# Kernel tuning notes

Hardware: AMD Instinct MI355X
Metric: run time of the kernel (lower is better)

Reference implementation:

```python
import jax, jax.numpy as jnp
import numpy as np

MAX_ITER = 10
EPS = 1e-4


def setup_inputs() -> dict:
    key = jax.random.key(0)
    k1, k2, k3 = jax.random.split(key, 3)
    B, N, M = 64, 1024, 1024
    s = jax.random.uniform(k1, (B, N, M), dtype=jnp.float32)
    nrows = jax.random.randint(k2, (B,), 0, N, dtype=jnp.int64 if jax.config.read('jax_enable_x64') else jnp.int32)
    ncols = jax.random.randint(k3, (B,), 0, M, dtype=nrows.dtype)
    return {"s": s, "nrows": nrows, "ncols": ncols}


def _sinkhorn(s, nrows, ncols):
    # Faithful to torch Sinkhorn.forward with exp=False, dummy_row=False.
    # The torch code builds [B,N,N]/[B,M,M] block-of-ones matrices and matmuls;
    # mathematically this is a masked column-sum (even iters) / row-sum (odd iters)
    # over the valid nrows[b] x ncols[b] block, followed by division inside the
    # block and zeroing outside it.
    B, N, M = s.shape
    row_mask = jnp.arange(N)[None, :] < nrows[:, None]            # [B, N]
    col_mask = jnp.arange(M)[None, :] < ncols[:, None]            # [B, M]
    mask = row_mask[:, :, None] & col_mask[:, None, :]            # [B, N, M]

    out = s + EPS
    for i in range(MAX_ITER):
        if i % 2 == 0:
            # column sums over valid rows -> [B, 1, M]
            sm = jnp.sum(jnp.where(row_mask[:, :, None], out, 0.0), axis=1, keepdims=True)
        else:
            # row sums over valid cols -> [B, N, 1]
            sm = jnp.sum(jnp.where(col_mask[:, None, :], out, 0.0), axis=2, keepdims=True)
        sm = jnp.where(sm == 0, 1.0, sm)  # guard (only affects masked-out entries)
        out = jnp.where(mask, out / sm, 0.0)
    return out


def reference(s, nrows, ncols):
    return _sinkhorn(s, nrows, ncols)
```

## Files before the change

kernel.cpp:

```cpp
#include <hip/hip_runtime.h>

#define EPS 1e-4f
constexpr int N_DIM = 1024;
constexpr int M_DIM = 1024;
constexpr int BATCH = 64;


template <bool FIRST, int CHUNKS>
__global__ __launch_bounds__(256)
void col_sweep(const float* __restrict__ s,
               const int* __restrict__ nrows,
               const int* __restrict__ ncols,
               const float* __restrict__ u,
               float* __restrict__ tpart) {
    const int b  = blockIdx.y;
    const int mt = blockIdx.x & 3;
    const int ch = blockIdx.x >> 2;
    const int R = nrows[b], C = ncols[b];
    const int lane = threadIdx.x & 63, wv = threadIdx.x >> 6;
    const int m0 = mt * 256;
    const int m  = m0 + lane * 4;

    constexpr int ROWS = N_DIM / CHUNKS;
    const int n0 = ch * ROWS;
    const int nend = min(R, n0 + ROWS);

    __shared__ float rlds[1024];
    if (!FIRST) {
        for (int i = threadIdx.x; i < ROWS; i += 256) {
            float uu = u[b * N_DIM + n0 + i];
            rlds[i] = (uu == 0.f) ? 1.f : 1.f / uu;
        }
        __syncthreads();
    }

    float4 acc = make_float4(0.f, 0.f, 0.f, 0.f);
    if (m0 < C) {
        const float* __restrict__ sb = s + (size_t)b * N_DIM * M_DIM;
#pragma unroll 4
        for (int n = n0 + wv; n < nend; n += 4) {
            float4 v = *(const float4*)(sb + (size_t)n * M_DIM + m);
            float rn = FIRST ? 1.f : rlds[n - n0];
            acc.x += rn * (v.x + EPS);
            acc.y += rn * (v.y + EPS);
            acc.z += rn * (v.z + EPS);
            acc.w += rn * (v.w + EPS);
        }
    }

    __shared__ float4 red[4][64];
    red[wv][lane] = acc;
    __syncthreads();
    if (wv == 0) {
        float4 a0 = red[0][lane], a1 = red[1][lane],
               a2 = red[2][lane], a3 = red[3][lane];
        float4 t = make_float4(a0.x + a1.x + a2.x + a3.x,
                               a0.y + a1.y + a2.y + a3.y,
                               a0.z + a1.z + a2.z + a3.z,
                               a0.w + a1.w + a2.w + a3.w);
        *(float4*)(tpart + ((size_t)(ch * BATCH + b)) * M_DIM + m) = t;
    }
}

template <int CHUNKS, bool WRITE_C>
__global__ __launch_bounds__(256)
void row_sweep(const float* __restrict__ s,
               const int* __restrict__ nrows,
               const int* __restrict__ ncols,
               const float* __restrict__ tpart,
               float* __restrict__ u,
               float* __restrict__ cOut) {
    const int b = blockIdx.y;
    const int R = nrows[b], C = ncols[b];
    const int n0 = blockIdx.x * 16;
    if (n0 >= R) return;

    __shared__ float clds[M_DIM];
    {
        const int t4 = threadIdx.x;
        float4 sum = make_float4(0.f, 0.f, 0.f, 0.f);
#pragma unroll
        for (int ch = 0; ch < CHUNKS; ++ch) {
            float4 p = *(const float4*)(tpart + ((size_t)(ch * BATCH + b)) * M_DIM + t4 * 4);
            sum.x += p.x; sum.y += p.y; sum.z += p.z; sum.w += p.w;
        }
        float4 cv;
        cv.x = (sum.x == 0.f) ? 1.f : 1.f / sum.x;
        cv.y = (sum.y == 0.f) ? 1.f : 1.f / sum.y;
        cv.z = (sum.z == 0.f) ? 1.f : 1.f / sum.z;
        cv.w = (sum.w == 0.f) ? 1.f : 1.f / sum.w;
        *(float4*)&clds[t4 * 4] = cv;
        if (WRITE_C && blockIdx.x == 0)
            *(float4*)(cOut + b * M_DIM + t4 * 4) = cv;
    }
    __syncthreads();

    const int lane = threadIdx.x & 63, wv = threadIdx.x >> 6;
    const int C4 = C >> 2;
#pragma unroll
    for (int i = 0; i < 4; ++i) {
        const int n = n0 + wv * 4 + i;
        if (n >= R) break;
        const float* __restrict__ srow = s + ((size_t)b * N_DIM + n) * M_DIM;
        float sum = 0.f;
        for (int j = lane; j < C4; j += 64) {
            float4 v  = ((const float4*)srow)[j];
            float4 cc = *(const float4*)&clds[j * 4];
            sum += (v.x + EPS) * cc.x + (v.y + EPS) * cc.y +
                   (v.z + EPS) * cc.z + (v.w + EPS) * cc.w;
        }
        for (int mm = (C4 << 2) + lane; mm < C; mm += 64)
            sum += (srow[mm] + EPS) * clds[mm];
#pragma unroll
        for (int off = 32; off; off >>= 1) sum += __shfl_down(sum, off);
        if (lane == 0) u[b * N_DIM + n] = sum;
    }
}

__global__ __launch_bounds__(256)
void finalize(const float* __restrict__ s,
              const int* __restrict__ nrows,
              const int* __restrict__ ncols,
              const float* __restrict__ u,
              const float* __restrict__ c,
              float* __restrict__ out) {
    const int n = blockIdx.x;
    const int b = blockIdx.y;
    const int R = nrows[b], C = ncols[b];
    const size_t base = ((size_t)b * N_DIM + n) * M_DIM;
    const int m = threadIdx.x * 4;

    float4 o = make_float4(0.f, 0.f, 0.f, 0.f);
    if (n < R && m < C) {
        float uu = u[b * N_DIM + n];
        float rn = (uu == 0.f) ? 1.f : 1.f / uu;
        float4 v  = *(const float4*)(s + base + m);
        float4 cc = *(const float4*)(c + b * M_DIM + m);
        o.x = (m + 0 < C) ? (v.x + EPS) * rn * cc.x : 0.f;
        o.y = (m + 1 < C) ? (v.y + EPS) * rn * cc.y : 0.f;
        o.z = (m + 2 < C) ? (v.z + EPS) * rn * cc.z : 0.f;
        o.w = (m + 3 < C) ? (v.w + EPS) * rn * cc.w : 0.f;
    }
    *(float4*)(out + base + m) = o;
}

extern "C" void kernel_launch(void* const* d_in, const int* in_sizes, int n_in,
                              void* d_out, int out_size, void* d_ws, size_t ws_size,
                              hipStream_t stream) {
    const float* s     = (const float*)d_in[0];
    const int*   nrows = (const int*)d_in[1];
    const int*   ncols = (const int*)d_in[2];
    float*       out   = (float*)d_out;

    const size_t needed4 = (size_t)(4 * BATCH * M_DIM + BATCH * N_DIM + BATCH * M_DIM) * 4;
    const bool big = ws_size >= needed4;

    if (big) {
        constexpr int CH = 4;
        float* tpart = (float*)d_ws;
        float* u = tpart + (size_t)CH * BATCH * M_DIM;
        float* c = u + (size_t)BATCH * N_DIM;
        dim3 colGrid(4 * CH, BATCH), rowGrid(64, BATCH);
        col_sweep<true, CH><<<colGrid, 256, 0, stream>>>(s, nrows, ncols, u, tpart);
        row_sweep<CH, false><<<rowGrid, 256, 0, stream>>>(s, nrows, ncols, tpart, u, c);
        for (int k = 1; k < 4; ++k) {
            col_sweep<false, CH><<<colGrid, 256, 0, stream>>>(s, nrows, ncols, u, tpart);
            row_sweep<CH, false><<<rowGrid, 256, 0, stream>>>(s, nrows, ncols, tpart, u, c);
        }
        col_sweep<false, CH><<<colGrid, 256, 0, stream>>>(s, nrows, ncols, u, tpart);
        row_sweep<CH, true><<<rowGrid, 256, 0, stream>>>(s, nrows, ncols, tpart, u, c);
        finalize<<<dim3(N_DIM, BATCH), 256, 0, stream>>>(s, nrows, ncols, u, c, out);
    } else {
        constexpr int CH = 1;
        float* tpart = (float*)d_ws;
        float* u = tpart + (size_t)CH * BATCH * M_DIM;
        float* c = u + (size_t)BATCH * N_DIM;
        dim3 colGrid(4 * CH, BATCH), rowGrid(64, BATCH);
        col_sweep<true, CH><<<colGrid, 256, 0, stream>>>(s, nrows, ncols, u, tpart);
        row_sweep<CH, false><<<rowGrid, 256, 0, stream>>>(s, nrows, ncols, tpart, u, c);
        for (int k = 1; k < 4; ++k) {
            col_sweep<false, CH><<<colGrid, 256, 0, stream>>>(s, nrows, ncols, u, tpart);
            row_sweep<CH, false><<<rowGrid, 256, 0, stream>>>(s, nrows, ncols, tpart, u, c);
        }
        col_sweep<false, CH><<<colGrid, 256, 0, stream>>>(s, nrows, ncols, u, tpart);
        row_sweep<CH, true><<<rowGrid, 256, 0, stream>>>(s, nrows, ncols, tpart, u, c);
        finalize<<<dim3(N_DIM, BATCH), 256, 0, stream>>>(s, nrows, ncols, u, c, out);
    }
}
```

Baseline: 244.3 us.

## Cache fp16 copy of masked input and run Sinkhorn sweeps on it

The first column sweep adds EPS, masks columns, and writes a half-precision copy of the input into the workspace. All later row and column sweeps read this fp16 copy instead of the fp32 input, halving the bytes per sweep. Row blocks and column blocks are widened to 8 elements per lane. The cost is an extra write pass, a large workspace requirement, and fp16 rounding error in the normalisation sums.

```diff
diff --git a/kernel.cpp b/kernel.cpp
--- a/kernel.cpp
+++ b/kernel.cpp
@@ -1,17 +1,216 @@
 #include <hip/hip_runtime.h>
+#include <hip/hip_fp16.h>
 
 #define EPS 1e-4f
 constexpr int N_DIM = 1024;
 constexpr int M_DIM = 1024;
 constexpr int BATCH = 64;
-
+constexpr int CH    = 4;
+constexpr int ROWS  = N_DIM / CH;
+
+
+
+__global__ __launch_bounds__(256)
+void col_first_conv(const float* __restrict__ s,
+                    const int* __restrict__ nrows,
+                    const int* __restrict__ ncols,
+                    __half* __restrict__ h,
+                    float* __restrict__ tpart) {
+    const int b  = blockIdx.y;
+    const int mt = blockIdx.x & 3;
+    const int ch = blockIdx.x >> 2;
+    const int R = nrows[b], C = ncols[b];
+    const int lane = threadIdx.x & 63, wv = threadIdx.x >> 6;
+    const int m = mt * 256 + lane * 4;
+    const int n0 = ch * ROWS;
+    const int nend = min(R, n0 + ROWS);
+    const size_t base = (size_t)b * N_DIM * M_DIM;
+
+    float4 acc = make_float4(0.f, 0.f, 0.f, 0.f);
+    if (mt * 256 < C) {
+        for (int n = n0 + wv; n < nend; n += 4) {
+            float4 v = *(const float4*)(s + base + (size_t)n * M_DIM + m);
+            v.x = (m + 0 < C) ? v.x + EPS : 0.f;
+            v.y = (m + 1 < C) ? v.y + EPS : 0.f;
+            v.z = (m + 2 < C) ? v.z + EPS : 0.f;
+            v.w = (m + 3 < C) ? v.w + EPS : 0.f;
+            acc.x += v.x; acc.y += v.y; acc.z += v.z; acc.w += v.w;
+            union { __half2 h2[2]; uint2 u2; } pk;
+            pk.h2[0] = __floats2half2_rn(v.x, v.y);
+            pk.h2[1] = __floats2half2_rn(v.z, v.w);
+            *(uint2*)(h + base + (size_t)n * M_DIM + m) = pk.u2;
+        }
+    } else {
+        const uint2 z = make_uint2(0u, 0u);
+        for (int n = n0 + wv; n < nend; n += 4)
+            *(uint2*)(h + base + (size_t)n * M_DIM + m) = z;
+    }
+    __shared__ float4 red[4][64];
+    red[wv][lane] = acc;
+    __syncthreads();
+    if (wv == 0) {
+        float4 a0 = red[0][lane], a1 = red[1][lane],
+               a2 = red[2][lane], a3 = red[3][lane];
+        float4 t = make_float4(a0.x + a1.x + a2.x + a3.x,
+                               a0.y + a1.y + a2.y + a3.y,
+                               a0.z + a1.z + a2.z + a3.z,
+                               a0.w + a1.w + a2.w + a3.w);
+        *(float4*)(tpart + (size_t)(ch * BATCH + b) * M_DIM + m) = t;
+    }
+}
+
+__global__ __launch_bounds__(256)
+void col_h(const __half* __restrict__ h,
+           const int* __restrict__ nrows,
+           const int* __restrict__ ncols,
+           const float* __restrict__ u,
+           float* __restrict__ tpart) {
+    const int b  = blockIdx.y;
+    const int mt = blockIdx.x & 1;
+    const int ch = blockIdx.x >> 1;
+    const int R = nrows[b], C = ncols[b];
+    const int lane = threadIdx.x & 63, wv = threadIdx.x >> 6;
+    const int m = mt * 512 + lane * 8;
+    const int n0 = ch * ROWS;
+    const int nend = min(R, n0 + ROWS);
+    const size_t base = (size_t)b * N_DIM * M_DIM;
+
+    __shared__ float rlds[ROWS];
+    {
+        float uu = u[b * N_DIM + n0 + threadIdx.x];
+        rlds[threadIdx.x] = (uu == 0.f) ? 1.f : 1.f / uu;
+    }
+    __syncthreads();
+
+    float acc[8] = {0.f, 0.f, 0.f, 0.f, 0.f, 0.f, 0.f, 0.f};
+    if (mt * 512 < C) {
+        for (int n = n0 + wv; n < nend; n += 4) {
+            uint4 raw = *(const uint4*)(h + base + (size_t)n * M_DIM + m);
+            const float rn = rlds[n - n0];
+            const __half2* hp = (const __half2*)&raw;
+#pragma unroll
+            for (int k = 0; k < 4; ++k) {
+                float2 f = __half22float2(hp[k]);
+                acc[2 * k]     += rn * f.x;
+                acc[2 * k + 1] += rn * f.y;
+            }
+        }
+    }
+    __shared__ float red[4][64 * 8];
+#pragma unroll
+    for (int k = 0; k < 8; ++k) red[wv][lane * 8 + k] = acc[k];
+    __syncthreads();
+    if (wv == 0) {
+        float t[8];
+#pragma unroll
+        for (int k = 0; k < 8; ++k)
+            t[k] = red[0][lane * 8 + k] + red[1][lane * 8 + k] +
+                   red[2][lane * 8 + k] + red[3][lane * 8 + k];
+        float* tp = tpart + (size_t)(ch * BATCH + b) * M_DIM + m;
+        *(float4*)tp       = make_float4(t[0], t[1], t[2], t[3]);
+        *(float4*)(tp + 4) = make_float4(t[4], t[5], t[6], t[7]);
+    }
+}
+
+template <bool WRITE_C>
+__global__ __launch_bounds__(256)
+void row_h(const __half* __restrict__ h,
+           const int* __restrict__ nrows,
+           const int* __restrict__ ncols,
+           const float* __restrict__ tpart,
+           float* __restrict__ u,
+           float* __restrict__ cOut) {
+    const int b = blockIdx.y;
+    const int R = nrows[b], C = ncols[b];
+    const int n0 = blockIdx.x * 32;
+    if (n0 >= R) return;
+    const size_t base = (size_t)b * N_DIM * M_DIM;
+
+    __shared__ float clds[M_DIM];
+    {
+        const int t4 = threadIdx.x * 4;
+        float4 sum = make_float4(0.f, 0.f, 0.f, 0.f);
+#pragma unroll
+        for (int ch = 0; ch < CH; ++ch) {
+            float4 p = *(const float4*)(tpart + (size_t)(ch * BATCH + b) * M_DIM + t4);
+            sum.x += p.x; sum.y += p.y; sum.z += p.z; sum.w += p.w;
+        }
+        float4 cv;
+        cv.x = (sum.x == 0.f) ? 1.f : 1.f / sum.x;
+        cv.y = (sum.y == 0.f) ? 1.f : 1.f / sum.y;
+        cv.z = (sum.z == 0.f) ? 1.f : 1.f / sum.z;
+        cv.w = (sum.w == 0.f) ? 1.f : 1.f / sum.w;
+        *(float4*)&clds[t4] = cv;
+        if (WRITE_C && blockIdx.x == 0)
+            *(float4*)(cOut + b * M_DIM + t4) = cv;
+    }
+    __syncthreads();
+
+    const int lane = threadIdx.x & 63, wv = threadIdx.x >> 6;
+    const bool hi = (C > 512);
+#pragma unroll 2
+    for (int i = 0; i < 8; ++i) {
+        const int n = n0 + wv * 8 + i;
+        if (n >= R) break;
+        const __half* hrow = h + base + (size_t)n * M_DIM;
+        float sum = 0.f;
+        {
+            uint4 raw = *(const uint4*)(hrow + lane * 8);
+            const __half2* hp = (const __half2*)&raw;
+            const float* cl = &clds[lane * 8];
+#pragma unroll
+            for (int k = 0; k < 4; ++k) {
+                float2 f = __half22float2(hp[k]);
+                sum += f.x * cl[2 * k] + f.y * cl[2 * k + 1];
+            }
+        }
+        if (hi) {
+            uint4 raw = *(const uint4*)(hrow + 512 + lane * 8);
+            const __half2* hp = (const __half2*)&raw;
+            const float* cl = &clds[512 + lane * 8];
+#pragma unroll
+            for (int k = 0; k < 4; ++k) {
+                float2 f = __half22float2(hp[k]);
+                sum += f.x * cl[2 * k] + f.y * cl[2 * k + 1];
+            }
+        }
+#pragma unroll
+        for (int off = 32; off; off >>= 1) sum += __shfl_down(sum, off);
+        if (lane == 0) u[b * N_DIM + n] = sum;
+    }
+}
+
+__global__ __launch_bounds__(256)
+void finalize(const float* __restrict__ s,
+              const int* __restrict__ nrows,
+              const int* __restrict__ ncols,
+              const float* __restrict__ u,
+              const float* __restrict__ c,
+              float* __restrict__ out) {
+    const int n = blockIdx.x;
+    const int b = blockIdx.y;
+    const int R = nrows[b], C = ncols[b];
+    const size_t base = ((size_t)b * N_DIM + n) * M_DIM;
+    const int m = threadIdx.x * 4;
+
+    float4 o = make_float4(0.f, 0.f, 0.f, 0.f);
+    if (n < R && m < C) {
+        float uu = u[b * N_DIM + n];
+        float rn = (uu == 0.f) ? 1.f : 1.f / uu;
+        float4 v  = *(const float4*)(s + base + m);
+        float4 cc = *(const float4*)(c + b * M_DIM + m);
+        o.x = (m + 0 < C) ? (v.x + EPS) * rn * cc.x : 0.f;
+        o.y = (m + 1 < C) ? (v.y + EPS) * rn * cc.y : 0.f;
+        o.z = (m + 2 < C) ? (v.z + EPS) * rn * cc.z : 0.f;
+        o.w = (m + 3 < C) ? (v.w + EPS) * rn * cc.w : 0.f;
+    }
+    *(float4*)(out + base + m) = o;
+}
 
 template <bool FIRST, int CHUNKS>
 __global__ __launch_bounds__(256)
-void col_sweep(const float* __restrict__ s,
-               const int* __restrict__ nrows,
-               const int* __restrict__ ncols,
-               const float* __restrict__ u,
+void col_sweep(const float* __restrict__ s, const int* __restrict__ nrows,
+               const int* __restrict__ ncols, const float* __restrict__ u,
                float* __restrict__ tpart) {
     const int b  = blockIdx.y;
     const int mt = blockIdx.x & 3;
@@ -20,20 +219,18 @@
     const int lane = threadIdx.x & 63, wv = threadIdx.x >> 6;
     const int m0 = mt * 256;
     const int m  = m0 + lane * 4;
-
-    constexpr int ROWS = N_DIM / CHUNKS;
-    const int n0 = ch * ROWS;
-    const int nend = min(R, n0 + ROWS);
-
-    __shared__ float rlds[1024];
+    constexpr int RW = N_DIM / CHUNKS;
+    const int n0 = ch * RW;
+    const int nend = min(R, n0 + RW);
+
+    __shared__ float rlds[RW > 1024 ? 1 : RW];
     if (!FIRST) {
-        for (int i = threadIdx.x; i < ROWS; i += 256) {
+        for (int i = threadIdx.x; i < RW; i += 256) {
             float uu = u[b * N_DIM + n0 + i];
             rlds[i] = (uu == 0.f) ? 1.f : 1.f / uu;
         }
         __syncthreads();
     }
-
     float4 acc = make_float4(0.f, 0.f, 0.f, 0.f);
     if (m0 < C) {
         const float* __restrict__ sb = s + (size_t)b * N_DIM * M_DIM;
@@ -41,40 +238,31 @@
         for (int n = n0 + wv; n < nend; n += 4) {
             float4 v = *(const float4*)(sb + (size_t)n * M_DIM + m);
             float rn = FIRST ? 1.f : rlds[n - n0];
-            acc.x += rn * (v.x + EPS);
-            acc.y += rn * (v.y + EPS);
-            acc.z += rn * (v.z + EPS);
-            acc.w += rn * (v.w + EPS);
-        }
-    }
-
+            acc.x += rn * (v.x + EPS); acc.y += rn * (v.y + EPS);
+            acc.z += rn * (v.z + EPS); acc.w += rn * (v.w + EPS);
+        }
+    }
     __shared__ float4 red[4][64];
     red[wv][lane] = acc;
     __syncthreads();
     if (wv == 0) {
         float4 a0 = red[0][lane], a1 = red[1][lane],
                a2 = red[2][lane], a3 = red[3][lane];
-        float4 t = make_float4(a0.x + a1.x + a2.x + a3.x,
-                               a0.y + a1.y + a2.y + a3.y,
-                               a0.z + a1.z + a2.z + a3.z,
-                               a0.w + a1.w + a2.w + a3.w);
+        float4 t = make_float4(a0.x + a1.x + a2.x + a3.x, a0.y + a1.y + a2.y + a3.y,
+                               a0.z + a1.z + a2.z + a3.z, a0.w + a1.w + a2.w + a3.w);
         *(float4*)(tpart + ((size_t)(ch * BATCH + b)) * M_DIM + m) = t;
     }
 }
 
 template <int CHUNKS, bool WRITE_C>
 __global__ __launch_bounds__(256)
-void row_sweep(const float* __restrict__ s,
-               const int* __restrict__ nrows,
-               const int* __restrict__ ncols,
-               const float* __restrict__ tpart,
-               float* __restrict__ u,
-               float* __restrict__ cOut) {
+void row_sweep(const float* __restrict__ s, const int* __restrict__ nrows,
+               const int* __restrict__ ncols, const float* __restrict__ tpart,
+               float* __restrict__ u, float* __restrict__ cOut) {
     const int b = blockIdx.y;
     const int R = nrows[b], C = ncols[b];
     const int n0 = blockIdx.x * 16;
     if (n0 >= R) return;
-
     __shared__ float clds[M_DIM];
     {
         const int t4 = threadIdx.x;
@@ -94,7 +282,6 @@
             *(float4*)(cOut + b * M_DIM + t4 * 4) = cv;
     }
     __syncthreads();
-
     const int lane = threadIdx.x & 63, wv = threadIdx.x >> 6;
     const int C4 = C >> 2;
 #pragma unroll
@@ -117,33 +304,6 @@
     }
 }
 
-__global__ __launch_bounds__(256)
-void finalize(const float* __restrict__ s,
-              const int* __restrict__ nrows,
-              const int* __restrict__ ncols,
-              const float* __restrict__ u,
-              const float* __restrict__ c,
-              float* __restrict__ out) {
-    const int n = blockIdx.x;
-    const int b = blockIdx.y;
-    const int R = nrows[b], C = ncols[b];
-    const size_t base = ((size_t)b * N_DIM + n) * M_DIM;
-    const int m = threadIdx.x * 4;
-
-    float4 o = make_float4(0.f, 0.f, 0.f, 0.f);
-    if (n < R && m < C) {
-        float uu = u[b * N_DIM + n];
-        float rn = (uu == 0.f) ? 1.f : 1.f / uu;
-        float4 v  = *(const float4*)(s + base + m);
-        float4 cc = *(const float4*)(c + b * M_DIM + m);
-        o.x = (m + 0 < C) ? (v.x + EPS) * rn * cc.x : 0.f;
-        o.y = (m + 1 < C) ? (v.y + EPS) * rn * cc.y : 0.f;
-        o.z = (m + 2 < C) ? (v.z + EPS) * rn * cc.z : 0.f;
-        o.w = (m + 3 < C) ? (v.w + EPS) * rn * cc.w : 0.f;
-    }
-    *(float4*)(out + base + m) = o;
-}
-
 extern "C" void kernel_launch(void* const* d_in, const int* in_sizes, int n_in,
                               void* d_out, int out_size, void* d_ws, size_t ws_size,
                               hipStream_t stream) {
@@ -152,38 +312,60 @@
     const int*   ncols = (const int*)d_in[2];
     float*       out   = (float*)d_out;
 
-    const size_t needed4 = (size_t)(4 * BATCH * M_DIM + BATCH * N_DIM + BATCH * M_DIM) * 4;
-    const bool big = ws_size >= needed4;
-
-    if (big) {
-        constexpr int CH = 4;
+    const size_t hElems   = (size_t)BATCH * N_DIM * M_DIM;
+    const size_t need_f16 = hElems * 2 +
+                            ((size_t)CH * BATCH * M_DIM + BATCH * N_DIM + BATCH * M_DIM) * 4;
+
+    if (ws_size >= need_f16) {
+        __half* h     = (__half*)d_ws;
+        float*  tpart = (float*)(h + hElems);
+        float*  u     = tpart + (size_t)CH * BATCH * M_DIM;
+        float*  c     = u + (size_t)BATCH * N_DIM;
+
+        dim3 colGrid1(4 * CH, BATCH);
+        dim3 colGridH(2 * CH, BATCH);
+        dim3 rowGridH(32, BATCH);
+
+        col_first_conv<<<colGrid1, 256, 0, stream>>>(s, nrows, ncols, h, tpart);
+        row_h<false><<<rowGridH, 256, 0, stream>>>(h, nrows, ncols, tpart, u, c);
+        for (int k = 0; k < 3; ++k) {
+            col_h<<<colGridH, 256, 0, stream>>>(h, nrows, ncols, u, tpart);
+            row_h<false><<<rowGridH, 256, 0, stream>>>(h, nrows, ncols, tpart, u, c);
+        }
+        col_h<<<colGridH, 256, 0, stream>>>(h, nrows, ncols, u, tpart);
+        row_h<true><<<rowGridH, 256, 0, stream>>>(h, nrows, ncols, tpart, u, c);
+        finalize<<<dim3(N_DIM, BATCH), 256, 0, stream>>>(s, nrows, ncols, u, c, out);
+        return;
+    }
+
+    const size_t need4 = (size_t)(4 * BATCH * M_DIM + BATCH * N_DIM + BATCH * M_DIM) * 4;
+    if (ws_size >= need4) {
         float* tpart = (float*)d_ws;
-        float* u = tpart + (size_t)CH * BATCH * M_DIM;
+        float* u = tpart + (size_t)4 * BATCH * M_DIM;
         float* c = u + (size_t)BATCH * N_DIM;
-        dim3 colGrid(4 * CH, BATCH), rowGrid(64, BATCH);
-        col_sweep<true, CH><<<colGrid, 256, 0, stream>>>(s, nrows, ncols, u, tpart);
-        row_sweep<CH, false><<<rowGrid, 256, 0, stream>>>(s, nrows, ncols, tpart, u, c);
+        dim3 colGrid(16, BATCH), rowGrid(64, BATCH);
+        col_sweep<true, 4><<<colGrid, 256, 0, stream>>>(s, nrows, ncols, u, tpart);
+        row_sweep<4, false><<<rowGrid, 256, 0, stream>>>(s, nrows, ncols, tpart, u, c);
         for (int k = 1; k < 4; ++k) {
-            col_sweep<false, CH><<<colGrid, 256, 0, stream>>>(s, nrows, ncols, u, tpart);
-            row_sweep<CH, false><<<rowGrid, 256, 0, stream>>>(s, nrows, ncols, tpart, u, c);
-        }
-        col_sweep<false, CH><<<colGrid, 256, 0, stream>>>(s, nrows, ncols, u, tpart);
-        row_sweep<CH, true><<<rowGrid, 256, 0, stream>>>(s, nrows, ncols, tpart, u, c);
+            col_sweep<false, 4><<<colGrid, 256, 0, stream>>>(s, nrows, ncols, u, tpart);
+            row_sweep<4, false><<<rowGrid, 256, 0, stream>>>(s, nrows, ncols, tpart, u, c);
+        }
+        col_sweep<false, 4><<<colGrid, 256, 0, stream>>>(s, nrows, ncols, u, tpart);
+        row_sweep<4, true><<<rowGrid, 256, 0, stream>>>(s, nrows, ncols, tpart, u, c);
         finalize<<<dim3(N_DIM, BATCH), 256, 0, stream>>>(s, nrows, ncols, u, c, out);
     } else {
-        constexpr int CH = 1;
         float* tpart = (float*)d_ws;
-        float* u = tpart + (size_t)CH * BATCH * M_DIM;
+        float* u = tpart + (size_t)BATCH * M_DIM;
         float* c = u + (size_t)BATCH * N_DIM;
-        dim3 colGrid(4 * CH, BATCH), rowGrid(64, BATCH);
-        col_sweep<true, CH><<<colGrid, 256, 0, stream>>>(s, nrows, ncols, u, tpart);
-        row_sweep<CH, false><<<rowGrid, 256, 0, stream>>>(s, nrows, ncols, tpart, u, c);
+        dim3 colGrid(4, BATCH), rowGrid(64, BATCH);
+        col_sweep<true, 1><<<colGrid, 256, 0, stream>>>(s, nrows, ncols, u, tpart);
+        row_sweep<1, false><<<rowGrid, 256, 0, stream>>>(s, nrows, ncols, tpart, u, c);
         for (int k = 1; k < 4; ++k) {
-            col_sweep<false, CH><<<colGrid, 256, 0, stream>>>(s, nrows, ncols, u, tpart);
-            row_sweep<CH, false><<<rowGrid, 256, 0, stream>>>(s, nrows, ncols, tpart, u, c);
-        }
-        col_sweep<false, CH><<<colGrid, 256, 0, stream>>>(s, nrows, ncols, u, tpart);
-        row_sweep<CH, true><<<rowGrid, 256, 0, stream>>>(s, nrows, ncols, tpart, u, c);
+            col_sweep<false, 1><<<colGrid, 256, 0, stream>>>(s, nrows, ncols, u, tpart);
+            row_sweep<1, false><<<rowGrid, 256, 0, stream>>>(s, nrows, ncols, tpart, u, c);
+        }
+        col_sweep<false, 1><<<colGrid, 256, 0, stream>>>(s, nrows, ncols, u, tpart);
+        row_sweep<1, true><<<rowGrid, 256, 0, stream>>>(s, nrows, ncols, tpart, u, c);
         finalize<<<dim3(N_DIM, BATCH), 256, 0, stream>>>(s, nrows, ncols, u, c, out);
     }
 }
```

New measurement: 267.6 us. 9.5% more time.
